# Performance work log

Measured on AMD Instinct MI355X. Metric: run time of the kernel, lower is better.

## Reference

```python
import jax, jax.numpy as jnp
import numpy as np

B, H, S, D = 2, 16, 2048, 64

def setup_inputs() -> dict:
    key = jax.random.key(0)
    kq, kk, kv, km = jax.random.split(key, 4)
    q = jax.random.normal(kq, (B, H, S, D), dtype=jnp.float32)
    k = jax.random.normal(kk, (B, H, S, D), dtype=jnp.float32)
    v = jax.random.normal(kv, (B, H, S, D), dtype=jnp.float32)
    mask = jax.random.randint(km, (B, 1, S, S), 0, 2, dtype=jnp.int32)
    return {"q": q, "k": k, "v": v, "mask": mask}

def reference(q, k, v, mask):
    d_k = q.shape[-1]
    # scores: [B, H, S, S]
    scores = jnp.einsum('bhqd,bhkd->bhqk', q, k) / jnp.sqrt(jnp.float32(d_k))
    scores = jnp.where(mask == 0, -jnp.inf, scores)
    attn = jax.nn.softmax(scores, axis=-1)
    return jnp.einsum('bhqk,bhkd->bhqd', attn, v)
```

## Files before the change

### kernel.cpp

```cpp
#include <hip/hip_runtime.h>
#include <hip/hip_bf16.h>

typedef unsigned short u16;
typedef unsigned int   u32;
typedef unsigned long long u64;
typedef __attribute__((ext_vector_type(8)))  __bf16 bf16x8;
typedef __attribute__((ext_vector_type(4)))  float  f32x4;
typedef __attribute__((ext_vector_type(16))) float  f32x16;
typedef __attribute__((ext_vector_type(8)))  u16    ushort8;
typedef __attribute__((ext_vector_type(4)))  u32    u32x4;

#define S_LEN 2048
#define D_DIM 64
#define NBH   32
#define SD    131072
#define MROW  32
#define MB_PB 65536
#define NT    32

#define FR_BH 131072

#define KF_OFF 0u
#define VF_OFF 8388608u
#define MB_OFF 16777216u
#define WS_NEED 17833984u

#define QSCALE 0.18033688011112042f

static __device__ __forceinline__ u16 f2bf(float f) {
  u32 u = __builtin_bit_cast(u32, f);
  u += 0x7fffu + ((u >> 16) & 1u);
  return (u16)(u >> 16);
}

static __device__ __forceinline__ void gl16(const void* g, void* l) {
  __builtin_amdgcn_global_load_lds(
      (const __attribute__((address_space(1))) u32*)g,
      (__attribute__((address_space(3))) u32*)l, 16, 0, 0);
}

static __device__ __forceinline__ u32 cvtpk(float lo, float hi) {
  u32 d;
  asm("v_cvt_pk_bf16_f32 %0, %1, %2" : "=v"(d) : "v"(lo), "v"(hi));
  return d;
}
static __device__ __forceinline__ void plswap(u32& a, u32& b) {
  asm volatile("v_permlane32_swap_b32 %0, %1" : "+v"(a), "+v"(b));
}

#define WAITV(N) asm volatile("s_waitcnt vmcnt(" #N ")" ::: "memory")

__global__ __launch_bounds__(256) void prep_all(
    const float* __restrict__ K, const float* __restrict__ V, const int* __restrict__ M,
    u16* __restrict__ Kf, u16* __restrict__ Vf, u64* __restrict__ Mb) {
  const int bx = blockIdx.x, tid = threadIdx.x;
  if (bx < 2048) {
    __shared__ u16 t[64][72];
    const bool isK = bx < 1024;
    const int idx = isK ? bx : bx - 1024;
    const int bh = idx >> 5, tt = idx & 31;
    const float* src = (isK ? K : V) + ((size_t)bh * S_LEN + tt * 64) * D_DIM;
    const int r = tid >> 2, c0 = (tid & 3) * 16;
#pragma unroll
    for (int i = 0; i < 16; i += 4) {
      float4 x = *reinterpret_cast<const float4*>(src + r * 64 + c0 + i);
      t[r][c0+i]   = f2bf(x.x); t[r][c0+i+1] = f2bf(x.y);
      t[r][c0+i+2] = f2bf(x.z); t[r][c0+i+3] = f2bf(x.w);
    }
    __syncthreads();
    u16* dst = (isK ? Kf : Vf) + (size_t)bh * FR_BH + (size_t)tt * 4096;
#pragma unroll
    for (int qq = 0; qq < 2; ++qq) {
      const int f = tid * 2 + qq;
      const int sp = f >> 7, half = (f >> 6) & 1, l = f & 63;
      ushort8 u;
      if (isK) {
        u = *reinterpret_cast<const ushort8*>(&t[half * 32 + (l & 31)][sp * 16 + (l >> 5) * 8]);
      } else {
        const int kv0 = sp * 16 + (l >> 5) * 8, d = half * 32 + (l & 31);
#pragma unroll
        for (int j = 0; j < 8; ++j) u[j] = t[kv0 + j][d];
      }
      *reinterpret_cast<ushort8*>(dst + (size_t)f * 8) = u;
    }
  } else {
    int g = (bx - 2048) * 256 + tid;
    int lane = g & 63;
    int v = M[(size_t)g];
    u64 bits = __ballot(v != 0);
    if (lane == 0) Mb[g >> 6] = bits;
  }
}

static __device__ __forceinline__ void iter_body(
    const u16* kb, const u16* vb, u64 mw,
    const bf16x8* Qf, f32x16& accOT0, f32x16& accOT1, float& l_,
    int lane, int hi) {
  const u32 mlo = (u32)mw, mhiw = (u32)(mw >> 32);

  f32x16 sT0 = {0,0,0,0,0,0,0,0,0,0,0,0,0,0,0,0};
  f32x16 sT1 = {0,0,0,0,0,0,0,0,0,0,0,0,0,0,0,0};
  __builtin_amdgcn_s_setprio(1);
#pragma unroll
  for (int s = 0; s < 4; ++s) {
    bf16x8 k0 = *reinterpret_cast<const bf16x8*>(kb + s * 1024 + lane * 8);
    bf16x8 k1 = *reinterpret_cast<const bf16x8*>(kb + s * 1024 + 512 + lane * 8);
    sT0 = __builtin_amdgcn_mfma_f32_32x32x16_bf16(k0, Qf[s], sT0, 0, 0, 0);
    sT1 = __builtin_amdgcn_mfma_f32_32x32x16_bf16(k1, Qf[s], sT1, 0, 0, 0);
  }
  __builtin_amdgcn_s_setprio(0);

  float lp0 = 0.f, lp1 = 0.f;
  u32 A0_[8], A1_[8];
#pragma unroll
  for (int T = 0; T < 2; ++T) {
    const f32x16& sv = T ? sT1 : sT0;
    const u32 mword = T ? mhiw : mlo;
#pragma unroll
    for (int j = 0; j < 8; ++j) {
      const int r0 = 2 * j, r1 = 2 * j + 1;
      const int b0 = (r0 & 3) + 8 * (r0 >> 2) + 4 * hi;
      const int b1 = (r1 & 3) + 8 * (r1 >> 2) + 4 * hi;
      float e0 = __builtin_amdgcn_exp2f(sv[r0]);
      float e1 = __builtin_amdgcn_exp2f(sv[r1]);
      int s0 = __builtin_amdgcn_sbfe(mword, b0, 1);
      int s1 = __builtin_amdgcn_sbfe(mword, b1, 1);
      e0 = __builtin_bit_cast(float, __builtin_bit_cast(u32, e0) & (u32)s0);
      e1 = __builtin_bit_cast(float, __builtin_bit_cast(u32, e1) & (u32)s1);
      lp0 += e0; lp1 += e1;
      u32 w = cvtpk(e0, e1);
      if (T == 0) A0_[j] = w; else A1_[j] = w;
    }
  }
  l_ += lp0 + lp1;

  bf16x8 PA[4];
  {
    u32 a, c, b2, d2;
    a = A0_[0]; c = A0_[2]; plswap(a, c);
    b2 = A0_[1]; d2 = A0_[3]; plswap(b2, d2);
    u32x4 w0 = {a, b2, c, d2}; PA[0] = __builtin_bit_cast(bf16x8, w0);
    a = A0_[4]; c = A0_[6]; plswap(a, c);
    b2 = A0_[5]; d2 = A0_[7]; plswap(b2, d2);
    u32x4 w1 = {a, b2, c, d2}; PA[1] = __builtin_bit_cast(bf16x8, w1);
    a = A1_[0]; c = A1_[2]; plswap(a, c);
    b2 = A1_[1]; d2 = A1_[3]; plswap(b2, d2);
    u32x4 w2 = {a, b2, c, d2}; PA[2] = __builtin_bit_cast(bf16x8, w2);
    a = A1_[4]; c = A1_[6]; plswap(a, c);
    b2 = A1_[5]; d2 = A1_[7]; plswap(b2, d2);
    u32x4 w3 = {a, b2, c, d2}; PA[3] = __builtin_bit_cast(bf16x8, w3);
  }

  __builtin_amdgcn_s_setprio(1);
#pragma unroll
  for (int ks = 0; ks < 4; ++ks) {
    bf16x8 v0 = *reinterpret_cast<const bf16x8*>(vb + ks * 1024 + lane * 8);
    bf16x8 v1 = *reinterpret_cast<const bf16x8*>(vb + ks * 1024 + 512 + lane * 8);
    accOT0 = __builtin_amdgcn_mfma_f32_32x32x16_bf16(v0, PA[ks], accOT0, 0, 0, 0);
    accOT1 = __builtin_amdgcn_mfma_f32_32x32x16_bf16(v1, PA[ks], accOT1, 0, 0, 0);
  }
  __builtin_amdgcn_s_setprio(0);
}

__global__ __launch_bounds__(256, 2) void attn_fwd9(
    const float* __restrict__ Q, const u16* __restrict__ Kf,
    const u16* __restrict__ Vf, const u64* __restrict__ Mb,
    float* __restrict__ O) {
  __shared__ __align__(16) u16 LB[32768];

  const int tid  = threadIdx.x;
  const int lane = tid & 63;
  const int wid  = tid >> 6;
  const int l31  = lane & 31;
  const int hi   = lane >> 5;

  const int bh = blockIdx.y, b = bh >> 4;
  const int q0w = blockIdx.x * 128 + wid * 32;
  const size_t base = (size_t)bh * SD;

  bf16x8 Qf[4];
  {
    const float* qsrc = Q + base + (size_t)(q0w + l31) * 64;
#pragma unroll
    for (int s = 0; s < 4; ++s) {
      const int d0 = s * 16 + hi * 8;
      float4 x = *reinterpret_cast<const float4*>(qsrc + d0);
      float4 y = *reinterpret_cast<const float4*>(qsrc + d0 + 4);
      u32x4 w;
      w[0] = cvtpk(x.x * QSCALE, x.y * QSCALE);
      w[1] = cvtpk(x.z * QSCALE, x.w * QSCALE);
      w[2] = cvtpk(y.x * QSCALE, y.y * QSCALE);
      w[3] = cvtpk(y.z * QSCALE, y.w * QSCALE);
      Qf[s] = __builtin_bit_cast(bf16x8, w);
    }
  }

  const u16* kfA = Kf + (size_t)bh * FR_BH;
  const u16* vfA = Vf + (size_t)bh * FR_BH;

  const u64* mp = Mb + (size_t)b * MB_PB + (size_t)(q0w + l31) * MROW;

  f32x16 accOT0 = {0,0,0,0,0,0,0,0,0,0,0,0,0,0,0,0};
  f32x16 accOT1 = {0,0,0,0,0,0,0,0,0,0,0,0,0,0,0,0};
  float l_ = 0.f;

#define STAGE(buf, it) do {                                                                  \
    gl16(kfA + (size_t)(it) * 4096 + tid * 8,        LB + (buf) * 4096 + tid * 8);           \
    gl16(kfA + (size_t)(it) * 4096 + 2048 + tid * 8, LB + (buf) * 4096 + 2048 + tid * 8);    \
    gl16(vfA + (size_t)(it) * 4096 + tid * 8,        LB + 16384 + (buf) * 4096 + tid * 8);   \
    gl16(vfA + (size_t)(it) * 4096 + 2048 + tid * 8, LB + 16384 + (buf) * 4096 + 2048 + tid * 8); \
  } while (0)

#define BODY(IT, J, WN, DOSTAGE) do {                                    \
    WAITV(WN);                                                            \
    __builtin_amdgcn_s_barrier();                                         \
    __builtin_amdgcn_sched_barrier(0);                                    \
    if (DOSTAGE) { STAGE((((J) + 3) & 3), (IT) + 3); }                    \
    iter_body(LB + (J) * 4096, LB + 16384 + (J) * 4096, cm[J],            \
              Qf, accOT0, accOT1, l_, lane, hi);                          \
  } while (0)

  u64 cm[4], nm[4];
  cm[0] = mp[0]; cm[1] = mp[1]; cm[2] = mp[2]; cm[3] = mp[3];
  STAGE(0, 0); STAGE(1, 1); STAGE(2, 2);

#pragma unroll 1
  for (int g = 0; g < 7; ++g) {
    const int it0 = g * 4;
    nm[0] = mp[it0 + 4]; nm[1] = mp[it0 + 5];
    nm[2] = mp[it0 + 6]; nm[3] = mp[it0 + 7];
    BODY(it0 + 0, 0, 8, true);
    BODY(it0 + 1, 1, 8, true);
    BODY(it0 + 2, 2, 8, true);
    BODY(it0 + 3, 3, 8, true);
    cm[0] = nm[0]; cm[1] = nm[1]; cm[2] = nm[2]; cm[3] = nm[3];
  }
  BODY(28, 0, 8, true);
  BODY(29, 1, 8, false);
  BODY(30, 2, 4, false);
  BODY(31, 3, 0, false);

  __syncthreads();

  l_ += __shfl_xor(l_, 32);
  const float inv = __builtin_amdgcn_rcpf(l_);

  float* Sc = (float*)((char*)LB + wid * 4608);
#pragma unroll
  for (int D0 = 0; D0 < 2; ++D0) {
    const f32x16& acc = D0 ? accOT1 : accOT0;
#pragma unroll
    for (int r = 0; r < 16; ++r) {
      const int dloc = (r & 3) + 8 * (r >> 2) + 4 * hi;
      Sc[l31 * 36 + dloc] = acc[r] * inv;
    }
    asm volatile("s_waitcnt lgkmcnt(0)" ::: "memory");
    __builtin_amdgcn_sched_barrier(0);
    const int qq = lane >> 1, off = (lane & 1) * 16;
#pragma unroll
    for (int j = 0; j < 4; ++j) {
      float4 x = *reinterpret_cast<const float4*>(&Sc[qq * 36 + off + j * 4]);
      *reinterpret_cast<float4*>(O + base + (size_t)(q0w + qq) * 64 + D0 * 32 + off + j * 4) = x;
    }
    asm volatile("s_waitcnt lgkmcnt(0)" ::: "memory");
    __builtin_amdgcn_sched_barrier(0);
  }
#undef STAGE
#undef BODY
}

#define KST 72
#define VST 40
#define PST 40
static __device__ __forceinline__ bf16x8 ld_frag(const u16* p) {
  ushort8 u = *reinterpret_cast<const ushort8*>(p);
  return __builtin_bit_cast(bf16x8, u);
}
__global__ __launch_bounds__(256) void attn_fwd_v1(
    const float* __restrict__ Q, const float* __restrict__ K,
    const float* __restrict__ V, const int* __restrict__ M,
    float* __restrict__ O) {
  __shared__ __align__(16) u16 Klds[32 * KST];
  __shared__ __align__(16) u16 Vlds[64 * VST];
  __shared__ __align__(16) u16 Plds[4 * 16 * PST];
  const int tid = threadIdx.x, lane = tid & 63, wid = tid >> 6;
  const int lrow = lane & 15, lgrp = lane >> 4;
  const int bh = blockIdx.y, b = bh >> 4;
  const int q0 = blockIdx.x * 64 + wid * 16;
  const int base = bh * S_LEN * D_DIM, mbase = b * S_LEN * S_LEN;
  bf16x8 qf[2];
#pragma unroll
  for (int c = 0; c < 2; ++c) {
    const float* src = Q + base + (q0 + lrow) * 64 + c * 32 + lgrp * 8;
    float4 x = *reinterpret_cast<const float4*>(src);
    float4 y = *reinterpret_cast<const float4*>(src + 4);
    ushort8 u;
    u[0]=f2bf(x.x*0.125f); u[1]=f2bf(x.y*0.125f); u[2]=f2bf(x.z*0.125f); u[3]=f2bf(x.w*0.125f);
    u[4]=f2bf(y.x*0.125f); u[5]=f2bf(y.y*0.125f); u[6]=f2bf(y.z*0.125f); u[7]=f2bf(y.w*0.125f);
    qf[c] = __builtin_bit_cast(bf16x8, u);
  }
  f32x4 accO[4];
#pragma unroll
  for (int c = 0; c < 4; ++c) accO[c] = (f32x4){0.f,0.f,0.f,0.f};
  float m_[4] = {-1e9f,-1e9f,-1e9f,-1e9f}, l_[4] = {0.f,0.f,0.f,0.f};
  const int srow = tid >> 3, scol = (tid & 7) * 8;
  for (int kv0 = 0; kv0 < S_LEN; kv0 += 32) {
    __syncthreads();
    {
      const float* src = K + base + (kv0 + srow) * 64 + scol;
      float4 x = *reinterpret_cast<const float4*>(src);
      float4 y = *reinterpret_cast<const float4*>(src + 4);
      ushort8 u;
      u[0]=f2bf(x.x); u[1]=f2bf(x.y); u[2]=f2bf(x.z); u[3]=f2bf(x.w);
      u[4]=f2bf(y.x); u[5]=f2bf(y.y); u[6]=f2bf(y.z); u[7]=f2bf(y.w);
      *reinterpret_cast<ushort8*>(&Klds[srow * KST + scol]) = u;
    }
    {
      const float* src = V + base + (kv0 + srow) * 64 + scol;
      float4 x = *reinterpret_cast<const float4*>(src);
      float4 y = *reinterpret_cast<const float4*>(src + 4);
      float vals[8] = {x.x,x.y,x.z,x.w,y.x,y.y,y.z,y.w};
#pragma unroll
      for (int i = 0; i < 8; ++i) Vlds[(scol + i) * VST + srow] = f2bf(vals[i]);
    }
    __syncthreads();
    f32x4 s0 = (f32x4){0.f,0.f,0.f,0.f}, s1 = (f32x4){0.f,0.f,0.f,0.f};
#pragma unroll
    for (int c = 0; c < 2; ++c) {
      bf16x8 k0 = ld_frag(&Klds[lrow * KST + c * 32 + lgrp * 8]);
      bf16x8 k1 = ld_frag(&Klds[(16 + lrow) * KST + c * 32 + lgrp * 8]);
      s0 = __builtin_amdgcn_mfma_f32_16x16x32_bf16(qf[c], k0, s0, 0, 0, 0);
      s1 = __builtin_amdgcn_mfma_f32_16x16x32_bf16(qf[c], k1, s1, 0, 0, 0);
    }
#pragma unroll
    for (int r = 0; r < 4; ++r) {
      const int moff = mbase + (q0 + lgrp * 4 + r) * S_LEN + kv0 + lrow;
      if (M[moff] == 0)      s0[r] = -1e30f;
      if (M[moff + 16] == 0) s1[r] = -1e30f;
    }
    const int pbase = wid * 16 * PST;
#pragma unroll
    for (int r = 0; r < 4; ++r) {
      float t = fmaxf(s0[r], s1[r]);
      t = fmaxf(t, __shfl_xor(t, 1)); t = fmaxf(t, __shfl_xor(t, 2));
      t = fmaxf(t, __shfl_xor(t, 4)); t = fmaxf(t, __shfl_xor(t, 8));
      float mn = fmaxf(m_[r], t);
      float sf = __expf(m_[r] - mn);
      m_[r] = mn;
      float p0 = __expf(s0[r] - mn), p1 = __expf(s1[r] - mn);
      float su = p0 + p1;
      su += __shfl_xor(su, 1); su += __shfl_xor(su, 2);
      su += __shfl_xor(su, 4); su += __shfl_xor(su, 8);
      l_[r] = l_[r] * sf + su;
      accO[0][r] *= sf; accO[1][r] *= sf; accO[2][r] *= sf; accO[3][r] *= sf;
      const int prow = lgrp * 4 + r;
      Plds[pbase + prow * PST + lrow]      = f2bf(p0);
      Plds[pbase + prow * PST + 16 + lrow] = f2bf(p1);
    }
    asm volatile("s_waitcnt lgkmcnt(0)" ::: "memory");
    __builtin_amdgcn_sched_barrier(0);
    bf16x8 pa = ld_frag(&Plds[pbase + lrow * PST + lgrp * 8]);
#pragma unroll
    for (int c = 0; c < 4; ++c) {
      bf16x8 bv = ld_frag(&Vlds[(c * 16 + lrow) * VST + lgrp * 8]);
      accO[c] = __builtin_amdgcn_mfma_f32_16x16x32_bf16(pa, bv, accO[c], 0, 0, 0);
    }
  }
#pragma unroll
  for (int r = 0; r < 4; ++r) {
    const float inv = 1.0f / l_[r];
    float* dst = O + base + (q0 + lgrp * 4 + r) * 64;
#pragma unroll
    for (int c = 0; c < 4; ++c) dst[c * 16 + lrow] = accO[c][r] * inv;
  }
}

extern "C" void kernel_launch(void* const* d_in, const int* in_sizes, int n_in,
                              void* d_out, int out_size, void* d_ws, size_t ws_size,
                              hipStream_t stream) {
  const float* q = (const float*)d_in[0];
  const float* k = (const float*)d_in[1];
  const float* v = (const float*)d_in[2];
  const int*   m = (const int*)d_in[3];
  float* out = (float*)d_out;

  if (ws_size < (size_t)WS_NEED) {
    dim3 grid(S_LEN / 64, NBH);
    attn_fwd_v1<<<grid, dim3(256), 0, stream>>>(q, k, v, m, out);
    return;
  }

  u16* Kf = (u16*)((char*)d_ws + KF_OFF);
  u16* Vf = (u16*)((char*)d_ws + VF_OFF);
  u64* Mb = (u64*)((char*)d_ws + MB_OFF);

  prep_all<<<dim3(34816), dim3(256), 0, stream>>>(k, v, m, Kf, Vf, Mb);
  attn_fwd9<<<dim3(S_LEN / 128, NBH), dim3(256), 0, stream>>>(q, Kf, Vf, Mb, out);
}
```

Measured before the change: 77.23 us.

## Split key range across two wave groups per block and merge partial outputs

The attention kernel now launches 512 threads per block. Two groups of four waves each process half of the key tiles for the same 128 queries, and their partial output accumulators and row sums are combined through shared memory before normalization. The 4-deep load pipeline with per-stage barriers becomes a per-group double buffer that waits for all outstanding loads each iteration. This raises wave-level parallelism and shortens each wave's serial loop, at the cost of less prefetch depth, full vmcnt(0) waits, and an extra LDS reduction.

```diff
diff --git a/kernel.cpp b/kernel.cpp
--- a/kernel.cpp
+++ b/kernel.cpp
@@ -48,7 +48,7 @@
   asm volatile("v_permlane32_swap_b32 %0, %1" : "+v"(a), "+v"(b));
 }
 
-#define WAITV(N) asm volatile("s_waitcnt vmcnt(" #N ")" ::: "memory")
+#define WAITV0 asm volatile("s_waitcnt vmcnt(0)" ::: "memory")
 
 __global__ __launch_bounds__(256) void prep_all(
     const float* __restrict__ K, const float* __restrict__ V, const int* __restrict__ M,
@@ -162,7 +162,7 @@
   __builtin_amdgcn_s_setprio(0);
 }
 
-__global__ __launch_bounds__(256, 2) void attn_fwd9(
+__global__ __launch_bounds__(512, 4) void attn_fwd10(
     const float* __restrict__ Q, const u16* __restrict__ Kf,
     const u16* __restrict__ Vf, const u64* __restrict__ Mb,
     float* __restrict__ O) {
@@ -171,11 +171,14 @@
   const int tid  = threadIdx.x;
   const int lane = tid & 63;
   const int wid  = tid >> 6;
+  const int grp  = wid >> 2;
+  const int gw   = wid & 3;
   const int l31  = lane & 31;
   const int hi   = lane >> 5;
+  const int ts   = tid & 255;
 
   const int bh = blockIdx.y, b = bh >> 4;
-  const int q0w = blockIdx.x * 128 + wid * 32;
+  const int q0w = blockIdx.x * 128 + gw * 32;
   const size_t base = (size_t)bh * SD;
 
   bf16x8 Qf[4];
@@ -195,78 +198,88 @@
     }
   }
 
+  u16* gK = LB + grp * 16384;
+  u16* gV = gK + 8192;
+
   const u16* kfA = Kf + (size_t)bh * FR_BH;
   const u16* vfA = Vf + (size_t)bh * FR_BH;
-
-  const u64* mp = Mb + (size_t)b * MB_PB + (size_t)(q0w + l31) * MROW;
+  const u64* mp  = Mb + (size_t)b * MB_PB + (size_t)(q0w + l31) * MROW;
 
   f32x16 accOT0 = {0,0,0,0,0,0,0,0,0,0,0,0,0,0,0,0};
   f32x16 accOT1 = {0,0,0,0,0,0,0,0,0,0,0,0,0,0,0,0};
   float l_ = 0.f;
 
-#define STAGE(buf, it) do {                                                                  \
-    gl16(kfA + (size_t)(it) * 4096 + tid * 8,        LB + (buf) * 4096 + tid * 8);           \
-    gl16(kfA + (size_t)(it) * 4096 + 2048 + tid * 8, LB + (buf) * 4096 + 2048 + tid * 8);    \
-    gl16(vfA + (size_t)(it) * 4096 + tid * 8,        LB + 16384 + (buf) * 4096 + tid * 8);   \
-    gl16(vfA + (size_t)(it) * 4096 + 2048 + tid * 8, LB + 16384 + (buf) * 4096 + 2048 + tid * 8); \
+#define STAGE(buf, tile) do {                                                      \
+    gl16(kfA + (size_t)(tile) * 4096 + ts * 8,        gK + (buf) * 4096 + ts * 8); \
+    gl16(kfA + (size_t)(tile) * 4096 + 2048 + ts * 8, gK + (buf) * 4096 + 2048 + ts * 8); \
+    gl16(vfA + (size_t)(tile) * 4096 + ts * 8,        gV + (buf) * 4096 + ts * 8); \
+    gl16(vfA + (size_t)(tile) * 4096 + 2048 + ts * 8, gV + (buf) * 4096 + 2048 + ts * 8); \
   } while (0)
 
-#define BODY(IT, J, WN, DOSTAGE) do {                                    \
-    WAITV(WN);                                                            \
-    __builtin_amdgcn_s_barrier();                                         \
-    __builtin_amdgcn_sched_barrier(0);                                    \
-    if (DOSTAGE) { STAGE((((J) + 3) & 3), (IT) + 3); }                    \
-    iter_body(LB + (J) * 4096, LB + 16384 + (J) * 4096, cm[J],            \
-              Qf, accOT0, accOT1, l_, lane, hi);                          \
-  } while (0)
-
-  u64 cm[4], nm[4];
-  cm[0] = mp[0]; cm[1] = mp[1]; cm[2] = mp[2]; cm[3] = mp[3];
-  STAGE(0, 0); STAGE(1, 1); STAGE(2, 2);
-
+  const int t0 = grp * 16;
+  STAGE(0, t0);
+  u64 cmCur = mp[t0];
+  WAITV0;
+  __builtin_amdgcn_s_barrier();
+
+  int buf = 0;
 #pragma unroll 1
-  for (int g = 0; g < 7; ++g) {
-    const int it0 = g * 4;
-    nm[0] = mp[it0 + 4]; nm[1] = mp[it0 + 5];
-    nm[2] = mp[it0 + 6]; nm[3] = mp[it0 + 7];
-    BODY(it0 + 0, 0, 8, true);
-    BODY(it0 + 1, 1, 8, true);
-    BODY(it0 + 2, 2, 8, true);
-    BODY(it0 + 3, 3, 8, true);
-    cm[0] = nm[0]; cm[1] = nm[1]; cm[2] = nm[2]; cm[3] = nm[3];
-  }
-  BODY(28, 0, 8, true);
-  BODY(29, 1, 8, false);
-  BODY(30, 2, 4, false);
-  BODY(31, 3, 0, false);
-
+  for (int it = 0; it < 16; ++it) {
+    u64 cmNext = 0;
+    if (it < 15) {
+      STAGE(buf ^ 1, t0 + it + 1);
+      cmNext = mp[t0 + it + 1];
+    }
+    iter_body(gK + buf * 4096, gV + buf * 4096, cmCur,
+              Qf, accOT0, accOT1, l_, lane, hi);
+    cmCur = cmNext;
+    WAITV0;
+    __builtin_amdgcn_s_barrier();
+    buf ^= 1;
+  }
+
+  l_ += __shfl_xor(l_, 32);
   __syncthreads();
-
-  l_ += __shfl_xor(l_, 32);
-  const float inv = __builtin_amdgcn_rcpf(l_);
-
-  float* Sc = (float*)((char*)LB + wid * 4608);
-#pragma unroll
-  for (int D0 = 0; D0 < 2; ++D0) {
-    const f32x16& acc = D0 ? accOT1 : accOT0;
-#pragma unroll
-    for (int r = 0; r < 16; ++r) {
-      const int dloc = (r & 3) + 8 * (r >> 2) + 4 * hi;
-      Sc[l31 * 36 + dloc] = acc[r] * inv;
-    }
-    asm volatile("s_waitcnt lgkmcnt(0)" ::: "memory");
-    __builtin_amdgcn_sched_barrier(0);
-    const int qq = lane >> 1, off = (lane & 1) * 16;
-#pragma unroll
-    for (int j = 0; j < 4; ++j) {
-      float4 x = *reinterpret_cast<const float4*>(&Sc[qq * 36 + off + j * 4]);
-      *reinterpret_cast<float4*>(O + base + (size_t)(q0w + qq) * 64 + D0 * 32 + off + j * 4) = x;
-    }
-    asm volatile("s_waitcnt lgkmcnt(0)" ::: "memory");
-    __builtin_amdgcn_sched_barrier(0);
+  float* P = (float*)((char*)LB + 24576);
+  const int pidx = (gw * 64 + lane) * 34;
+  if (grp == 1) {
+#pragma unroll
+    for (int r = 0; r < 16; ++r) P[pidx + r]      = accOT0[r];
+#pragma unroll
+    for (int r = 0; r < 16; ++r) P[pidx + 16 + r] = accOT1[r];
+    P[pidx + 32] = l_;
+  }
+  __syncthreads();
+  if (grp == 0) {
+#pragma unroll
+    for (int r = 0; r < 16; ++r) accOT0[r] += P[pidx + r];
+#pragma unroll
+    for (int r = 0; r < 16; ++r) accOT1[r] += P[pidx + 16 + r];
+    l_ += P[pidx + 32];
+
+    const float inv = __builtin_amdgcn_rcpf(l_);
+    float* sc = (float*)((char*)LB + gw * 4608);
+#pragma unroll
+    for (int D0 = 0; D0 < 2; ++D0) {
+      const f32x16& acc = D0 ? accOT1 : accOT0;
+#pragma unroll
+      for (int r = 0; r < 16; ++r) {
+        const int dloc = (r & 3) + 8 * (r >> 2) + 4 * hi;
+        sc[l31 * 36 + dloc] = acc[r] * inv;
+      }
+      asm volatile("s_waitcnt lgkmcnt(0)" ::: "memory");
+      __builtin_amdgcn_sched_barrier(0);
+      const int qq = lane >> 1, off = (lane & 1) * 16;
+#pragma unroll
+      for (int j = 0; j < 4; ++j) {
+        float4 x = *reinterpret_cast<const float4*>(&sc[qq * 36 + off + j * 4]);
+        *reinterpret_cast<float4*>(O + base + (size_t)(q0w + qq) * 64 + D0 * 32 + off + j * 4) = x;
+      }
+      asm volatile("s_waitcnt lgkmcnt(0)" ::: "memory");
+      __builtin_amdgcn_sched_barrier(0);
+    }
   }
 #undef STAGE
-#undef BODY
 }
 
 #define KST 72
@@ -395,5 +408,5 @@
   u64* Mb = (u64*)((char*)d_ws + MB_OFF);
 
   prep_all<<<dim3(34816), dim3(256), 0, stream>>>(k, v, m, Kf, Vf, Mb);
-  attn_fwd9<<<dim3(S_LEN / 128, NBH), dim3(256), 0, stream>>>(q, Kf, Vf, Mb, out);
-}
+  attn_fwd10<<<dim3(S_LEN / 128, NBH), dim3(512), 0, stream>>>(q, Kf, Vf, Mb, out);
+}
```

New measurement: 85.33 us. +10.5%, slower.

## Switch attention kernel to double-buffered LDS pipeline with higher occupancy

Applied to the files above, without the earlier changes.

Replaces the 4-buffer, 3-deep prefetch pipeline with a simple 2-buffer ping-pong that prefetches one tile ahead and fully drains vmcnt each iteration. LDS per block halves from 64KB to 32KB and launch bounds rise to 4 blocks per CU, so more waves can hide latency. The trade-off is a shallower prefetch depth and a full wait plus barrier every iteration, which may expose load latency if occupancy does not compensate. Register pressure also rises under the tighter launch bound.

```diff
diff --git a/kernel.cpp b/kernel.cpp
--- a/kernel.cpp
+++ b/kernel.cpp
@@ -48,7 +48,7 @@
   asm volatile("v_permlane32_swap_b32 %0, %1" : "+v"(a), "+v"(b));
 }
 
-#define WAITV(N) asm volatile("s_waitcnt vmcnt(" #N ")" ::: "memory")
+#define WAITV0 asm volatile("s_waitcnt vmcnt(0)" ::: "memory")
 
 __global__ __launch_bounds__(256) void prep_all(
     const float* __restrict__ K, const float* __restrict__ V, const int* __restrict__ M,
@@ -162,11 +162,11 @@
   __builtin_amdgcn_s_setprio(0);
 }
 
-__global__ __launch_bounds__(256, 2) void attn_fwd9(
+__global__ __launch_bounds__(256, 4) void attn_fwd12(
     const float* __restrict__ Q, const u16* __restrict__ Kf,
     const u16* __restrict__ Vf, const u64* __restrict__ Mb,
     float* __restrict__ O) {
-  __shared__ __align__(16) u16 LB[32768];
+  __shared__ __align__(16) u16 LB[16384];
 
   const int tid  = threadIdx.x;
   const int lane = tid & 63;
@@ -197,8 +197,7 @@
 
   const u16* kfA = Kf + (size_t)bh * FR_BH;
   const u16* vfA = Vf + (size_t)bh * FR_BH;
-
-  const u64* mp = Mb + (size_t)b * MB_PB + (size_t)(q0w + l31) * MROW;
+  const u64* mp  = Mb + (size_t)b * MB_PB + (size_t)(q0w + l31) * MROW;
 
   f32x16 accOT0 = {0,0,0,0,0,0,0,0,0,0,0,0,0,0,0,0};
   f32x16 accOT1 = {0,0,0,0,0,0,0,0,0,0,0,0,0,0,0,0};
@@ -207,38 +206,30 @@
 #define STAGE(buf, it) do {                                                                  \
     gl16(kfA + (size_t)(it) * 4096 + tid * 8,        LB + (buf) * 4096 + tid * 8);           \
     gl16(kfA + (size_t)(it) * 4096 + 2048 + tid * 8, LB + (buf) * 4096 + 2048 + tid * 8);    \
-    gl16(vfA + (size_t)(it) * 4096 + tid * 8,        LB + 16384 + (buf) * 4096 + tid * 8);   \
-    gl16(vfA + (size_t)(it) * 4096 + 2048 + tid * 8, LB + 16384 + (buf) * 4096 + 2048 + tid * 8); \
+    gl16(vfA + (size_t)(it) * 4096 + tid * 8,        LB + 8192 + (buf) * 4096 + tid * 8);    \
+    gl16(vfA + (size_t)(it) * 4096 + 2048 + tid * 8, LB + 8192 + (buf) * 4096 + 2048 + tid * 8); \
   } while (0)
 
-#define BODY(IT, J, WN, DOSTAGE) do {                                    \
-    WAITV(WN);                                                            \
-    __builtin_amdgcn_s_barrier();                                         \
-    __builtin_amdgcn_sched_barrier(0);                                    \
-    if (DOSTAGE) { STAGE((((J) + 3) & 3), (IT) + 3); }                    \
-    iter_body(LB + (J) * 4096, LB + 16384 + (J) * 4096, cm[J],            \
-              Qf, accOT0, accOT1, l_, lane, hi);                          \
-  } while (0)
-
-  u64 cm[4], nm[4];
-  cm[0] = mp[0]; cm[1] = mp[1]; cm[2] = mp[2]; cm[3] = mp[3];
-  STAGE(0, 0); STAGE(1, 1); STAGE(2, 2);
-
+  STAGE(0, 0);
+  u64 mwC = mp[0];
+  WAITV0;
+  __builtin_amdgcn_s_barrier();
+
+  int buf = 0;
 #pragma unroll 1
-  for (int g = 0; g < 7; ++g) {
-    const int it0 = g * 4;
-    nm[0] = mp[it0 + 4]; nm[1] = mp[it0 + 5];
-    nm[2] = mp[it0 + 6]; nm[3] = mp[it0 + 7];
-    BODY(it0 + 0, 0, 8, true);
-    BODY(it0 + 1, 1, 8, true);
-    BODY(it0 + 2, 2, 8, true);
-    BODY(it0 + 3, 3, 8, true);
-    cm[0] = nm[0]; cm[1] = nm[1]; cm[2] = nm[2]; cm[3] = nm[3];
-  }
-  BODY(28, 0, 8, true);
-  BODY(29, 1, 8, false);
-  BODY(30, 2, 4, false);
-  BODY(31, 3, 0, false);
+  for (int it = 0; it < NT; ++it) {
+    u64 mwN = 0;
+    if (it < NT - 1) {
+      STAGE(buf ^ 1, it + 1);
+      mwN = mp[it + 1];
+    }
+    iter_body(LB + buf * 4096, LB + 8192 + buf * 4096, mwC,
+              Qf, accOT0, accOT1, l_, lane, hi);
+    mwC = mwN;
+    WAITV0;
+    __builtin_amdgcn_s_barrier();
+    buf ^= 1;
+  }
 
   __syncthreads();
 
@@ -266,7 +257,6 @@
     __builtin_amdgcn_sched_barrier(0);
   }
 #undef STAGE
-#undef BODY
 }
 
 #define KST 72
@@ -395,5 +385,5 @@
   u64* Mb = (u64*)((char*)d_ws + MB_OFF);
 
   prep_all<<<dim3(34816), dim3(256), 0, stream>>>(k, v, m, Kf, Vf, Mb);
-  attn_fwd9<<<dim3(S_LEN / 128, NBH), dim3(256), 0, stream>>>(q, Kf, Vf, Mb, out);
-}
+  attn_fwd12<<<dim3(S_LEN / 128, NBH), dim3(256), 0, stream>>>(q, Kf, Vf, Mb, out);
+}
```

New measurement: 88.39 us. 1.14x slower.

## Split attention along key dimension into two halves with merge kernel

Applied to the files above, without the earlier changes.

Adds a split-K attention path. Each query tile is processed by two blocks, each covering half of the key tiles with a smaller double-buffered LDS footprint. Partial unnormalized outputs and row sums go to workspace, and a separate merge kernel adds them and normalizes. The aim is to double the grid (512 to 1024 blocks) so the GPU's CUs are better filled. In exchange it adds extra global writes and reads of partials plus one more kernel launch, and it only runs when the workspace is large enough. The merge of plain sums looks valid only because no running max is used, which the existing kernel also relies on.

```diff
diff --git a/kernel.cpp b/kernel.cpp
--- a/kernel.cpp
+++ b/kernel.cpp
@@ -23,7 +23,10 @@
 #define KF_OFF 0u
 #define VF_OFF 8388608u
 #define MB_OFF 16777216u
-#define WS_NEED 17833984u
+#define WS_NEED9 17833984u
+#define P_OFF  17825792u
+#define L_OFF  51380224u
+#define WS_NEED13 51904512u
 
 #define QSCALE 0.18033688011112042f
 
@@ -162,11 +165,11 @@
   __builtin_amdgcn_s_setprio(0);
 }
 
-__global__ __launch_bounds__(256, 2) void attn_fwd9(
+__global__ __launch_bounds__(256, 2) void attn_split(
     const float* __restrict__ Q, const u16* __restrict__ Kf,
     const u16* __restrict__ Vf, const u64* __restrict__ Mb,
-    float* __restrict__ O) {
-  __shared__ __align__(16) u16 LB[32768];
+    float* __restrict__ P, float* __restrict__ L) {
+  __shared__ __align__(16) u16 LB[16384];
 
   const int tid  = threadIdx.x;
   const int lane = tid & 63;
@@ -174,9 +177,12 @@
   const int l31  = lane & 31;
   const int hi   = lane >> 5;
 
+  const int qt    = blockIdx.x >> 1;
+  const int split = blockIdx.x & 1;
   const int bh = blockIdx.y, b = bh >> 4;
-  const int q0w = blockIdx.x * 128 + wid * 32;
+  const int q0w = qt * 128 + wid * 32;
   const size_t base = (size_t)bh * SD;
+  const int t0 = split * 16;
 
   bf16x8 Qf[4];
   {
@@ -197,8 +203,120 @@
 
   const u16* kfA = Kf + (size_t)bh * FR_BH;
   const u16* vfA = Vf + (size_t)bh * FR_BH;
-
-  const u64* mp = Mb + (size_t)b * MB_PB + (size_t)(q0w + l31) * MROW;
+  const u64* mp  = Mb + (size_t)b * MB_PB + (size_t)(q0w + l31) * MROW;
+
+  f32x16 accOT0 = {0,0,0,0,0,0,0,0,0,0,0,0,0,0,0,0};
+  f32x16 accOT1 = {0,0,0,0,0,0,0,0,0,0,0,0,0,0,0,0};
+  float l_ = 0.f;
+
+#define STAGE(buf, it) do {                                                                  \
+    gl16(kfA + (size_t)(it) * 4096 + tid * 8,        LB + (buf) * 4096 + tid * 8);           \
+    gl16(kfA + (size_t)(it) * 4096 + 2048 + tid * 8, LB + (buf) * 4096 + 2048 + tid * 8);    \
+    gl16(vfA + (size_t)(it) * 4096 + tid * 8,        LB + 8192 + (buf) * 4096 + tid * 8);    \
+    gl16(vfA + (size_t)(it) * 4096 + 2048 + tid * 8, LB + 8192 + (buf) * 4096 + 2048 + tid * 8); \
+  } while (0)
+
+  STAGE(0, t0); STAGE(1, t0 + 1);
+  u64 cm0 = mp[t0], cm1 = mp[t0 + 1];
+
+#pragma unroll 1
+  for (int t = 0; t < 8; ++t) {
+    WAITV(4);
+    __builtin_amdgcn_s_barrier();
+    __builtin_amdgcn_sched_barrier(0);
+    iter_body(LB, LB + 8192, cm0, Qf, accOT0, accOT1, l_, lane, hi);
+    __builtin_amdgcn_s_barrier();
+    if (t < 7) { STAGE(0, t0 + 2 * t + 2); cm0 = mp[t0 + 2 * t + 2]; }
+
+    WAITV(4);
+    __builtin_amdgcn_s_barrier();
+    __builtin_amdgcn_sched_barrier(0);
+    iter_body(LB + 4096, LB + 8192 + 4096, cm1, Qf, accOT0, accOT1, l_, lane, hi);
+    __builtin_amdgcn_s_barrier();
+    if (t < 7) { STAGE(1, t0 + 2 * t + 3); cm1 = mp[t0 + 2 * t + 3]; }
+  }
+
+  __syncthreads();
+
+  l_ += __shfl_xor(l_, 32);
+  const size_t prow = (size_t)(split * NBH + bh) * S_LEN;
+  if (hi == 0) L[prow + q0w + l31] = l_;
+
+  float* Sc = (float*)((char*)LB + wid * 4608);
+  float* Pd = P + prow * 64;
+#pragma unroll
+  for (int D0 = 0; D0 < 2; ++D0) {
+    const f32x16& acc = D0 ? accOT1 : accOT0;
+#pragma unroll
+    for (int r = 0; r < 16; ++r) {
+      const int dloc = (r & 3) + 8 * (r >> 2) + 4 * hi;
+      Sc[l31 * 36 + dloc] = acc[r];
+    }
+    asm volatile("s_waitcnt lgkmcnt(0)" ::: "memory");
+    __builtin_amdgcn_sched_barrier(0);
+    const int qq = lane >> 1, off = (lane & 1) * 16;
+#pragma unroll
+    for (int j = 0; j < 4; ++j) {
+      float4 x = *reinterpret_cast<const float4*>(&Sc[qq * 36 + off + j * 4]);
+      *reinterpret_cast<float4*>(Pd + (size_t)(q0w + qq) * 64 + D0 * 32 + off + j * 4) = x;
+    }
+    asm volatile("s_waitcnt lgkmcnt(0)" ::: "memory");
+    __builtin_amdgcn_sched_barrier(0);
+  }
+#undef STAGE
+}
+
+__global__ __launch_bounds__(256) void merge_k(
+    const float* __restrict__ P, const float* __restrict__ L,
+    float* __restrict__ O) {
+  const int gid = blockIdx.x * 256 + threadIdx.x;
+  const int row = gid >> 4;
+  const int c   = (gid & 15) * 4;
+  const float4 a = *reinterpret_cast<const float4*>(P + (size_t)row * 64 + c);
+  const float4 bq = *reinterpret_cast<const float4*>(P + 4194304ull + (size_t)row * 64 + c);
+  const float inv = __builtin_amdgcn_rcpf(L[row] + L[row + 65536]);
+  float4 o;
+  o.x = (a.x + bq.x) * inv; o.y = (a.y + bq.y) * inv;
+  o.z = (a.z + bq.z) * inv; o.w = (a.w + bq.w) * inv;
+  *reinterpret_cast<float4*>(O + (size_t)row * 64 + c) = o;
+}
+
+__global__ __launch_bounds__(256, 2) void attn_fwd9(
+    const float* __restrict__ Q, const u16* __restrict__ Kf,
+    const u16* __restrict__ Vf, const u64* __restrict__ Mb,
+    float* __restrict__ O) {
+  __shared__ __align__(16) u16 LB[32768];
+
+  const int tid  = threadIdx.x;
+  const int lane = tid & 63;
+  const int wid  = tid >> 6;
+  const int l31  = lane & 31;
+  const int hi   = lane >> 5;
+
+  const int bh = blockIdx.y, b = bh >> 4;
+  const int q0w = blockIdx.x * 128 + wid * 32;
+  const size_t base = (size_t)bh * SD;
+
+  bf16x8 Qf[4];
+  {
+    const float* qsrc = Q + base + (size_t)(q0w + l31) * 64;
+#pragma unroll
+    for (int s = 0; s < 4; ++s) {
+      const int d0 = s * 16 + hi * 8;
+      float4 x = *reinterpret_cast<const float4*>(qsrc + d0);
+      float4 y = *reinterpret_cast<const float4*>(qsrc + d0 + 4);
+      u32x4 w;
+      w[0] = cvtpk(x.x * QSCALE, x.y * QSCALE);
+      w[1] = cvtpk(x.z * QSCALE, x.w * QSCALE);
+      w[2] = cvtpk(y.x * QSCALE, y.y * QSCALE);
+      w[3] = cvtpk(y.z * QSCALE, y.w * QSCALE);
+      Qf[s] = __builtin_bit_cast(bf16x8, w);
+    }
+  }
+
+  const u16* kfA = Kf + (size_t)bh * FR_BH;
+  const u16* vfA = Vf + (size_t)bh * FR_BH;
+  const u64* mp  = Mb + (size_t)b * MB_PB + (size_t)(q0w + l31) * MROW;
 
   f32x16 accOT0 = {0,0,0,0,0,0,0,0,0,0,0,0,0,0,0,0};
   f32x16 accOT1 = {0,0,0,0,0,0,0,0,0,0,0,0,0,0,0,0};
@@ -384,7 +502,7 @@
   const int*   m = (const int*)d_in[3];
   float* out = (float*)d_out;
 
-  if (ws_size < (size_t)WS_NEED) {
+  if (ws_size < (size_t)WS_NEED9) {
     dim3 grid(S_LEN / 64, NBH);
     attn_fwd_v1<<<grid, dim3(256), 0, stream>>>(q, k, v, m, out);
     return;
@@ -395,5 +513,13 @@
   u64* Mb = (u64*)((char*)d_ws + MB_OFF);
 
   prep_all<<<dim3(34816), dim3(256), 0, stream>>>(k, v, m, Kf, Vf, Mb);
-  attn_fwd9<<<dim3(S_LEN / 128, NBH), dim3(256), 0, stream>>>(q, Kf, Vf, Mb, out);
-}
+
+  if (ws_size >= (size_t)WS_NEED13) {
+    float* P = (float*)((char*)d_ws + P_OFF);
+    float* L = (float*)((char*)d_ws + L_OFF);
+    attn_split<<<dim3(2 * S_LEN / 128, NBH), dim3(256), 0, stream>>>(q, Kf, Vf, Mb, P, L);
+    merge_k<<<dim3(4096), dim3(256), 0, stream>>>(P, L, out);
+  } else {
+    attn_fwd9<<<dim3(S_LEN / 128, NBH), dim3(256), 0, stream>>>(q, Kf, Vf, Mb, out);
+  }
+}
```

After: 90.42 us. +17.1%, slower.
